# Kernel tuning notes

Hardware: AMD Instinct MI355X
Metric: run time of the kernel (lower is better)

Reference implementation:

```python
import jax, jax.numpy as jnp
import numpy as np

H = 16
D_MODEL = 1024
D_K = D_MODEL // H
SEQ = 2048
BATCH = 2


def setup_inputs() -> dict:
    key = jax.random.key(0)
    ks = jax.random.split(key, 11)
    s = 1.0 / np.sqrt(D_MODEL)
    inp = {
        "query": jax.random.normal(ks[0], (SEQ, BATCH, D_MODEL), jnp.float32),
        "key_": jax.random.normal(ks[1], (SEQ, BATCH, D_MODEL), jnp.float32),
        "value": jax.random.normal(ks[2], (SEQ, BATCH, D_MODEL), jnp.float32),
        "Wq": jax.random.uniform(ks[3], (D_MODEL, D_MODEL), jnp.float32, -s, s),
        "bq": jax.random.uniform(ks[4], (D_MODEL,), jnp.float32, -s, s),
        "Wk": jax.random.uniform(ks[5], (D_MODEL, D_MODEL), jnp.float32, -s, s),
        "bk": jax.random.uniform(ks[6], (D_MODEL,), jnp.float32, -s, s),
        "Wv": jax.random.uniform(ks[7], (D_MODEL, D_MODEL), jnp.float32, -s, s),
        "bv": jax.random.uniform(ks[8], (D_MODEL,), jnp.float32, -s, s),
        "Wo": jax.random.uniform(ks[9], (D_MODEL, D_MODEL), jnp.float32, -s, s),
        "bo": jax.random.uniform(ks[10], (D_MODEL,), jnp.float32, -s, s),
    }
    return inp


def _mha(query, key_, value, Wq, bq, Wk, bk, Wv, bv, Wo, bo):
    S, B, D = query.shape
    # torch Linear: x @ W.T + b; then view(S,B,h,dk).transpose(0,2) -> [h,B,S,dk]
    def proj(x, W, b):
        return jnp.transpose((x @ W.T + b).reshape(S, B, H, D_K), (2, 1, 0, 3))

    q = proj(query, Wq, bq)   # [h, b, S, dk]
    k = proj(key_, Wk, bk)
    v = proj(value, Wv, bv)

    scores = jnp.einsum("hbqd,hbkd->hbqk", q, k) / jnp.sqrt(
        jnp.asarray(D_K, q.dtype)
    )  # [h, b, S, S]
    p_attn = jax.nn.softmax(scores, axis=-1)  # dropout p=0.0 -> identity
    x = jnp.einsum("hbqk,hbkd->hbqd", p_attn, v)  # [h, b, S, dk]
    x = jnp.transpose(x, (2, 1, 0, 3)).reshape(S, B, D)  # back to [S, B, D]
    return x @ Wo.T + bo


def reference(query, key_, value, Wq, bq, Wk, bk, Wv, bv, Wo, bo):
    return _mha(query, key_, value, Wq, bq, Wk, bk, Wv, bv, Wo, bo)
```

## Files before the change

kernel.cpp:

```cpp
#include <hip/hip_runtime.h>

#define SEQ   2048
#define BATCH 2
#define DM    1024
#define NH    16
#define DKD   64
#define MROWS (SEQ*BATCH)

#define QSCALE 0.18033688011112042f

using bf16x8 = __attribute__((ext_vector_type(8))) __bf16;
using bf16x4 = __attribute__((ext_vector_type(4))) __bf16;
using bf16x2 = __attribute__((ext_vector_type(2))) __bf16;
using f32x4  = __attribute__((ext_vector_type(4))) float;

__device__ __forceinline__ void gld_lds16(const __bf16* g, __bf16* l) {
  __builtin_amdgcn_global_load_lds(
      (__attribute__((address_space(1))) void*)(g),
      (__attribute__((address_space(3))) void*)(l), 16, 0, 0);
}

__global__ __launch_bounds__(256) void cvt_all(
    const float* __restrict__ s0, const float* __restrict__ s1,
    const float* __restrict__ s2, const float* __restrict__ s3,
    const float* __restrict__ s4, const float* __restrict__ s5,
    const float* __restrict__ s6,
    __bf16* __restrict__ d0, __bf16* __restrict__ d1, __bf16* __restrict__ d2,
    __bf16* __restrict__ d3, __bf16* __restrict__ d4, __bf16* __restrict__ d5,
    __bf16* __restrict__ d6, int n_big, int n_small) {
  int y = blockIdx.y;
  const float* s; __bf16* d;
  switch (y) {
    case 0: s = s0; d = d0; break;
    case 1: s = s1; d = d1; break;
    case 2: s = s2; d = d2; break;
    case 3: s = s3; d = d3; break;
    case 4: s = s4; d = d4; break;
    case 5: s = s5; d = d5; break;
    default: s = s6; d = d6; break;
  }
  int n = (y < 3) ? n_big : n_small;
  int i = (blockIdx.x * 256 + threadIdx.x) * 8;
  if (i >= n) return;
  const float4* sp = (const float4*)(s + i);
  float4 a = sp[0], b = sp[1];
  bf16x8 v;
  v[0]=(__bf16)a.x; v[1]=(__bf16)a.y; v[2]=(__bf16)a.z; v[3]=(__bf16)a.w;
  v[4]=(__bf16)b.x; v[5]=(__bf16)b.y; v[6]=(__bf16)b.z; v[7]=(__bf16)b.w;
  *(bf16x8*)(d + i) = v;
}

__device__ __forceinline__ void gemm_core(const __bf16* __restrict__ A,
                                          const __bf16* __restrict__ Bt,
                                          __bf16* Ash, __bf16* Bsh,
                                          f32x4 acc[4][4], int m0, int n0) {
  const int K = DM;
  int tid = threadIdx.x;
  int lane = tid & 63, quad = lane >> 4, l16 = lane & 15;
  int w = tid >> 6;
  int wm = (w & 1) * 64, wn = (w >> 1) * 64;
  for (int k0 = 0; k0 < K; k0 += 32) {
    __syncthreads();
#pragma unroll
    for (int it = 0; it < 2; ++it) {
      int c   = tid + it * 256;
      int row = c >> 2, ko = (c & 3) * 8;
      int base = (tid - lane + it * 256) * 8;
      gld_lds16(A  + (size_t)(m0 + row) * K + k0 + ko, Ash + base);
      gld_lds16(Bt + (size_t)(n0 + row) * K + k0 + ko, Bsh + base);
    }
    __syncthreads();
    bf16x8 af[4], bfr[4];
#pragma unroll
    for (int mi = 0; mi < 4; mi++)
      af[mi] = *(const bf16x8*)&Ash[(wm + mi * 16 + l16) * 32 + quad * 8];
#pragma unroll
    for (int ni = 0; ni < 4; ni++)
      bfr[ni] = *(const bf16x8*)&Bsh[(wn + ni * 16 + l16) * 32 + quad * 8];
#pragma unroll
    for (int mi = 0; mi < 4; mi++)
#pragma unroll
      for (int ni = 0; ni < 4; ni++)
        acc[mi][ni] = __builtin_amdgcn_mfma_f32_16x16x32_bf16(
            af[mi], bfr[ni], acc[mi][ni], 0, 0, 0);
  }
}

__global__ __launch_bounds__(256, 3) void gemm_qkv(
    const __bf16* __restrict__ Xq, const __bf16* __restrict__ Xk,
    const __bf16* __restrict__ Xv, const __bf16* __restrict__ Wqkv,
    const float* __restrict__ bqp, const float* __restrict__ bkp,
    const float* __restrict__ bvp,
    __bf16* __restrict__ Qb, __bf16* __restrict__ Kb, __bf16* __restrict__ Vt) {
  __shared__ __bf16 Ash[128 * 32], Bsh[128 * 32];
  __shared__ __bf16 Esh[4][16 * 72];
  int z = blockIdx.z;
  const __bf16* A   = (z == 0) ? Xq : (z == 1) ? Xk : Xv;
  const __bf16* Bt  = Wqkv + (size_t)z * (DM * DM);
  const float* bias = (z == 0) ? bqp : (z == 1) ? bkp : bvp;
  int m0 = blockIdx.y * 128, n0 = blockIdx.x * 128;
  f32x4 acc[4][4] = {};
  gemm_core(A, Bt, Ash, Bsh, acc, m0, n0);

  int tid = threadIdx.x, lane = tid & 63, quad = lane >> 4, l16 = lane & 15;
  int w = tid >> 6, wm = (w & 1) * 64, wn = (w >> 1) * 64;
  __bf16* E = Esh[w];
  int n_base = n0 + wn;
  int hh = n_base >> 6;
  float scale = (z == 0) ? QSCALE : 1.0f;
  float bb[4];
#pragma unroll
  for (int ni = 0; ni < 4; ni++) bb[ni] = bias[n_base + ni * 16 + l16] * scale;

  if (z == 2) {
#pragma unroll
    for (int ni = 0; ni < 4; ni++) {
#pragma unroll
      for (int mi = 0; mi < 4; mi++) {
        int s0 = mi * 8 + quad * 2;
        bf16x2 p0, p1;
        p0[0] = (__bf16)(acc[mi][ni][0] + bb[ni]);
        p0[1] = (__bf16)(acc[mi][ni][2] + bb[ni]);
        p1[0] = (__bf16)(acc[mi][ni][1] + bb[ni]);
        p1[1] = (__bf16)(acc[mi][ni][3] + bb[ni]);
        *(bf16x2*)&E[l16 * 72 + s0]      = p0;
        *(bf16x2*)&E[l16 * 72 + 32 + s0] = p1;
      }
      asm volatile("s_waitcnt lgkmcnt(0)" ::: "memory");
#pragma unroll
      for (int pass = 0; pass < 2; pass++) {
        int ddl = pass * 8 + (lane >> 3);
        int col = (lane & 7) * 8;
        bf16x8 v = *(const bf16x8*)&E[ddl * 72 + col];
        int b2 = col >> 5, sl = col & 31;
        int dd = ni * 16 + ddl;
        int sg = ((m0 + wm) >> 1) + sl;
        *(bf16x8*)&Vt[(((size_t)hh * BATCH + b2) * DKD + dd) * SEQ + sg] = v;
      }
      asm volatile("s_waitcnt lgkmcnt(0)" ::: "memory");
    }
  } else {
    __bf16* Out = (z == 0) ? Qb : Kb;
#pragma unroll
    for (int mi = 0; mi < 4; mi++) {
#pragma unroll
      for (int ni = 0; ni < 4; ni++)
#pragma unroll
        for (int r = 0; r < 4; r++)
          E[(quad * 4 + r) * 72 + ni * 16 + l16] =
              (__bf16)fmaf(acc[mi][ni][r], scale, bb[ni]);
      asm volatile("s_waitcnt lgkmcnt(0)" ::: "memory");
#pragma unroll
      for (int pass = 0; pass < 2; pass++) {
        int row16 = pass * 8 + (lane >> 3);
        int coll  = (lane & 7) * 8;
        bf16x8 v = *(const bf16x8*)&E[row16 * 72 + coll];
        int m = m0 + wm + mi * 16 + row16;
        int s = m >> 1, b2 = m & 1;
        *(bf16x8*)&Out[(((size_t)hh * BATCH + b2) * SEQ + s) * DKD + coll] = v;
      }
      asm volatile("s_waitcnt lgkmcnt(0)" ::: "memory");
    }
  }
}

__global__ __launch_bounds__(256, 3) void gemm_out(
    const __bf16* __restrict__ A, const __bf16* __restrict__ Bt,
    const float* __restrict__ bias, float* __restrict__ out) {
  __shared__ __bf16 Ash[64 * 32], Bsh[128 * 32];
  const int K = DM;
  int m0 = blockIdx.y * 64, n0 = blockIdx.x * 128;
  int tid = threadIdx.x;
  int lane = tid & 63, quad = lane >> 4, l16 = lane & 15;
  int w = tid >> 6;
  int wm = (w & 1) * 32, wn = (w >> 1) * 64;
  f32x4 acc[2][4] = {};
  for (int k0 = 0; k0 < K; k0 += 32) {
    __syncthreads();
    {
      int c = tid;
      int row = c >> 2, ko = (c & 3) * 8;
      gld_lds16(A + (size_t)(m0 + row) * K + k0 + ko,
                Ash + (tid - lane) * 8);
    }
#pragma unroll
    for (int it = 0; it < 2; ++it) {
      int c = tid + it * 256;
      int row = c >> 2, ko = (c & 3) * 8;
      gld_lds16(Bt + (size_t)(n0 + row) * K + k0 + ko,
                Bsh + (tid - lane + it * 256) * 8);
    }
    __syncthreads();
    bf16x8 af[2], bfr[4];
#pragma unroll
    for (int mi = 0; mi < 2; mi++)
      af[mi] = *(const bf16x8*)&Ash[(wm + mi * 16 + l16) * 32 + quad * 8];
#pragma unroll
    for (int ni = 0; ni < 4; ni++)
      bfr[ni] = *(const bf16x8*)&Bsh[(wn + ni * 16 + l16) * 32 + quad * 8];
#pragma unroll
    for (int mi = 0; mi < 2; mi++)
#pragma unroll
      for (int ni = 0; ni < 4; ni++)
        acc[mi][ni] = __builtin_amdgcn_mfma_f32_16x16x32_bf16(
            af[mi], bfr[ni], acc[mi][ni], 0, 0, 0);
  }
#pragma unroll
  for (int ni = 0; ni < 4; ni++) {
    int n = n0 + wn + ni * 16 + l16;
    float bb = bias[n];
#pragma unroll
    for (int mi = 0; mi < 2; mi++) {
#pragma unroll
      for (int r = 0; r < 4; r++) {
        int m = m0 + wm + mi * 16 + quad * 4 + r;
        out[(size_t)m * DM + n] = acc[mi][ni][r] + bb;
      }
    }
  }
}

__global__ __launch_bounds__(512, 4) void flash_attn(
    const __bf16* __restrict__ Qg, const __bf16* __restrict__ Kg,
    const __bf16* __restrict__ Vtg, __bf16* __restrict__ Xa) {
  __shared__ __bf16 Ksh[2][64 * 64];
  __shared__ __bf16 Vsh[2][64 * 64];
  __shared__ __bf16 Psh[8][16 * 64];
  int tid = threadIdx.x, w = tid >> 6, lane = tid & 63;
  int quad = lane >> 4, l16 = lane & 15, sw = l16 & 7;
  int n = blockIdx.x;
  int hb = n & 31, qi = n >> 5;
  int h = hb >> 1, b = hb & 1, q0 = qi * 128;
  size_t hboff = ((size_t)h * BATCH + b) * SEQ * DKD;
  const __bf16* Qp = Qg + hboff;
  const __bf16* Kp = Kg + hboff;
  const __bf16* Vp = Vtg + hboff;
  __bf16* Pw = Psh[w];

  bf16x8 qf[2];
#pragma unroll
  for (int kk = 0; kk < 2; kk++)
    qf[kk] = *(const bf16x8*)(
        Qp + (size_t)(q0 + w * 16 + l16) * DKD + kk * 32 + quad * 8);

  f32x4 o[4] = {};
  float l_ = 0.f;

  {
    int c = tid;
    int r = c >> 3, pp = c & 7;
    int off = (pp ^ (r & 7)) << 3;
    gld_lds16(Kp + (size_t)r * DKD + off, Ksh[0] + c * 8);
    gld_lds16(Vp + (size_t)r * SEQ + off, Vsh[0] + c * 8);
  }

  for (int t = 0; t < SEQ / 64; ++t) {
    __syncthreads();
    if (t + 1 < SEQ / 64) {
      int k0n = (t + 1) * 64, bn = (t + 1) & 1;
      int c = tid;
      int r = c >> 3, pp = c & 7;
      int off = (pp ^ (r & 7)) << 3;
      gld_lds16(Kp + (size_t)(k0n + r) * DKD + off, Ksh[bn] + c * 8);
      gld_lds16(Vp + (size_t)r * SEQ + k0n + off, Vsh[bn] + c * 8);
    }
    const __bf16* Kb_ = Ksh[t & 1];
    const __bf16* Vb_ = Vsh[t & 1];

    f32x4 sc[4];
#pragma unroll
    for (int ji = 0; ji < 4; ji++) {
      int rr = ji * 16 + l16;
      bf16x8 kf0 = *(const bf16x8*)&Kb_[rr * 64 + ((quad ^ sw) << 3)];
      bf16x8 kf1 = *(const bf16x8*)&Kb_[rr * 64 + (((4 + quad) ^ sw) << 3)];
      f32x4 t2 = {0.f, 0.f, 0.f, 0.f};
      t2 = __builtin_amdgcn_mfma_f32_16x16x32_bf16(kf0, qf[0], t2, 0, 0, 0);
      t2 = __builtin_amdgcn_mfma_f32_16x16x32_bf16(kf1, qf[1], t2, 0, 0, 0);
      sc[ji] = t2;
    }

#pragma unroll
    for (int ji = 0; ji < 4; ji++) {
      bf16x4 pk;
#pragma unroll
      for (int r = 0; r < 4; r++) {
        float pv = exp2f(sc[ji][r]);
        l_ += pv;
        pk[r] = (__bf16)pv;
      }
      *(bf16x4*)&Pw[l16 * 64 +
                    (((ji * 2 + (quad >> 1)) ^ sw) << 3) + ((quad & 1) << 2)] = pk;
    }

#pragma unroll
    for (int kk = 0; kk < 2; kk++) {
      bf16x8 pa = *(const bf16x8*)&Pw[l16 * 64 + (((kk * 4 + quad) ^ sw) << 3)];
#pragma unroll
      for (int ni = 0; ni < 4; ni++) {
        int rr = ni * 16 + l16;
        bf16x8 vb = *(const bf16x8*)&Vb_[rr * 64 + (((kk * 4 + quad) ^ sw) << 3)];
        o[ni] = __builtin_amdgcn_mfma_f32_16x16x32_bf16(pa, vb, o[ni], 0, 0, 0);
      }
    }
  }

  l_ += __shfl_xor(l_, 16, 64);
  l_ += __shfl_xor(l_, 32, 64);
  l_ = 1.0f / l_;
#pragma unroll
  for (int r = 0; r < 4; r++) {
    float li = __shfl(l_, quad * 4 + r, 64);
    int q = q0 + w * 16 + quad * 4 + r;
#pragma unroll
    for (int ni = 0; ni < 4; ni++) {
      int d = ni * 16 + l16;
      Xa[((size_t)q * BATCH + b) * DM + h * DKD + d] =
          (__bf16)(o[ni][r] * li);
    }
  }
}

extern "C" void kernel_launch(void* const* d_in, const int* in_sizes, int n_in,
                              void* d_out, int out_size, void* d_ws,
                              size_t ws_size, hipStream_t stream) {
  (void)in_sizes; (void)n_in; (void)out_size; (void)ws_size;
  const float* query = (const float*)d_in[0];
  const float* key_  = (const float*)d_in[1];
  const float* value = (const float*)d_in[2];
  const float* Wq = (const float*)d_in[3];
  const float* bq = (const float*)d_in[4];
  const float* Wk = (const float*)d_in[5];
  const float* bk = (const float*)d_in[6];
  const float* Wv = (const float*)d_in[7];
  const float* bv = (const float*)d_in[8];
  const float* Wo = (const float*)d_in[9];
  const float* bo = (const float*)d_in[10];

  const size_t NX = (size_t)MROWS * DM;
  const size_t NW = (size_t)DM * DM;
  __bf16* p    = (__bf16*)d_ws;
  __bf16* Xq   = p; p += NX;
  __bf16* Xk   = p; p += NX;
  __bf16* Xv   = p; p += NX;
  __bf16* Wqkv = p; p += 3 * NW;
  __bf16* Wob  = p; p += NW;
  __bf16* Qb   = p; p += NX;
  __bf16* Kb   = p; p += NX;
  __bf16* Vt   = p; p += NX;
  __bf16* Xa   = Xq;

  cvt_all<<<dim3((unsigned)(NX / 2048), 7), 256, 0, stream>>>(
      query, key_, value, Wq, Wk, Wv, Wo,
      Xq, Xk, Xv, Wqkv, Wqkv + NW, Wqkv + 2 * NW, Wob, (int)NX, (int)NW);

  gemm_qkv<<<dim3(DM / 128, MROWS / 128, 3), 256, 0, stream>>>(
      Xq, Xk, Xv, Wqkv, bq, bk, bv, Qb, Kb, Vt);
  flash_attn<<<dim3(512), 512, 0, stream>>>(Qb, Kb, Vt, Xa);
  gemm_out<<<dim3(DM / 128, MROWS / 64), 256, 0, stream>>>(
      Xa, Wob, bo, (float*)d_out);
}
```

Baseline: 228.6 us.

## Double GEMM K-tile to 64 with XOR-swizzled LDS; add setprio in attention

Both GEMM kernels now stage 64-wide K slices per iteration instead of 32. The LDS tiles use an XOR swizzle to avoid bank conflicts, and each slice runs two MFMA sub-steps. This halves the number of barriers and loop iterations per tile, but doubles the LDS footprint, which may limit occupancy. The flash attention kernel also wraps its MFMA phases in s_setprio and splits the row-sum accumulator into two, which shortens the dependency chain.

```diff
diff --git a/kernel.cpp b/kernel.cpp
--- a/kernel.cpp
+++ b/kernel.cpp
@@ -56,33 +56,39 @@
                                           f32x4 acc[4][4], int m0, int n0) {
   const int K = DM;
   int tid = threadIdx.x;
-  int lane = tid & 63, quad = lane >> 4, l16 = lane & 15;
+  int lane = tid & 63, quad = lane >> 4, l16 = lane & 15, sw = l16 & 7;
   int w = tid >> 6;
   int wm = (w & 1) * 64, wn = (w >> 1) * 64;
-  for (int k0 = 0; k0 < K; k0 += 32) {
-    __syncthreads();
-#pragma unroll
-    for (int it = 0; it < 2; ++it) {
+  for (int k0 = 0; k0 < K; k0 += 64) {
+    __syncthreads();
+#pragma unroll
+    for (int it = 0; it < 4; ++it) {
       int c   = tid + it * 256;
-      int row = c >> 2, ko = (c & 3) * 8;
+      int row = c >> 3, pp = c & 7;
+      int ko  = (pp ^ (row & 7)) << 3;
       int base = (tid - lane + it * 256) * 8;
       gld_lds16(A  + (size_t)(m0 + row) * K + k0 + ko, Ash + base);
       gld_lds16(Bt + (size_t)(n0 + row) * K + k0 + ko, Bsh + base);
     }
     __syncthreads();
-    bf16x8 af[4], bfr[4];
-#pragma unroll
-    for (int mi = 0; mi < 4; mi++)
-      af[mi] = *(const bf16x8*)&Ash[(wm + mi * 16 + l16) * 32 + quad * 8];
-#pragma unroll
-    for (int ni = 0; ni < 4; ni++)
-      bfr[ni] = *(const bf16x8*)&Bsh[(wn + ni * 16 + l16) * 32 + quad * 8];
-#pragma unroll
-    for (int mi = 0; mi < 4; mi++)
+#pragma unroll
+    for (int kk = 0; kk < 2; ++kk) {
+      bf16x8 af[4], bfr[4];
+#pragma unroll
+      for (int mi = 0; mi < 4; mi++)
+        af[mi] = *(const bf16x8*)&Ash[(wm + mi * 16 + l16) * 64 +
+                                      (((kk * 4 + quad) ^ sw) << 3)];
 #pragma unroll
       for (int ni = 0; ni < 4; ni++)
-        acc[mi][ni] = __builtin_amdgcn_mfma_f32_16x16x32_bf16(
-            af[mi], bfr[ni], acc[mi][ni], 0, 0, 0);
+        bfr[ni] = *(const bf16x8*)&Bsh[(wn + ni * 16 + l16) * 64 +
+                                       (((kk * 4 + quad) ^ sw) << 3)];
+#pragma unroll
+      for (int mi = 0; mi < 4; mi++)
+#pragma unroll
+        for (int ni = 0; ni < 4; ni++)
+          acc[mi][ni] = __builtin_amdgcn_mfma_f32_16x16x32_bf16(
+              af[mi], bfr[ni], acc[mi][ni], 0, 0, 0);
+    }
   }
 }
 
@@ -92,7 +98,7 @@
     const float* __restrict__ bqp, const float* __restrict__ bkp,
     const float* __restrict__ bvp,
     __bf16* __restrict__ Qb, __bf16* __restrict__ Kb, __bf16* __restrict__ Vt) {
-  __shared__ __bf16 Ash[128 * 32], Bsh[128 * 32];
+  __shared__ __bf16 Ash[128 * 64], Bsh[128 * 64];
   __shared__ __bf16 Esh[4][16 * 72];
   int z = blockIdx.z;
   const __bf16* A   = (z == 0) ? Xq : (z == 1) ? Xk : Xv;
@@ -167,43 +173,51 @@
 __global__ __launch_bounds__(256, 3) void gemm_out(
     const __bf16* __restrict__ A, const __bf16* __restrict__ Bt,
     const float* __restrict__ bias, float* __restrict__ out) {
-  __shared__ __bf16 Ash[64 * 32], Bsh[128 * 32];
+  __shared__ __bf16 Ash[64 * 64], Bsh[128 * 64];
   const int K = DM;
   int m0 = blockIdx.y * 64, n0 = blockIdx.x * 128;
   int tid = threadIdx.x;
-  int lane = tid & 63, quad = lane >> 4, l16 = lane & 15;
+  int lane = tid & 63, quad = lane >> 4, l16 = lane & 15, sw = l16 & 7;
   int w = tid >> 6;
   int wm = (w & 1) * 32, wn = (w >> 1) * 64;
   f32x4 acc[2][4] = {};
-  for (int k0 = 0; k0 < K; k0 += 32) {
-    __syncthreads();
-    {
-      int c = tid;
-      int row = c >> 2, ko = (c & 3) * 8;
-      gld_lds16(A + (size_t)(m0 + row) * K + k0 + ko,
-                Ash + (tid - lane) * 8);
-    }
+  for (int k0 = 0; k0 < K; k0 += 64) {
+    __syncthreads();
 #pragma unroll
     for (int it = 0; it < 2; ++it) {
       int c = tid + it * 256;
-      int row = c >> 2, ko = (c & 3) * 8;
+      int row = c >> 3, pp = c & 7;
+      int ko = (pp ^ (row & 7)) << 3;
+      gld_lds16(A + (size_t)(m0 + row) * K + k0 + ko,
+                Ash + (tid - lane + it * 256) * 8);
+    }
+#pragma unroll
+    for (int it = 0; it < 4; ++it) {
+      int c = tid + it * 256;
+      int row = c >> 3, pp = c & 7;
+      int ko = (pp ^ (row & 7)) << 3;
       gld_lds16(Bt + (size_t)(n0 + row) * K + k0 + ko,
                 Bsh + (tid - lane + it * 256) * 8);
     }
     __syncthreads();
-    bf16x8 af[2], bfr[4];
-#pragma unroll
-    for (int mi = 0; mi < 2; mi++)
-      af[mi] = *(const bf16x8*)&Ash[(wm + mi * 16 + l16) * 32 + quad * 8];
-#pragma unroll
-    for (int ni = 0; ni < 4; ni++)
-      bfr[ni] = *(const bf16x8*)&Bsh[(wn + ni * 16 + l16) * 32 + quad * 8];
-#pragma unroll
-    for (int mi = 0; mi < 2; mi++)
+#pragma unroll
+    for (int kk = 0; kk < 2; ++kk) {
+      bf16x8 af[2], bfr[4];
+#pragma unroll
+      for (int mi = 0; mi < 2; mi++)
+        af[mi] = *(const bf16x8*)&Ash[(wm + mi * 16 + l16) * 64 +
+                                      (((kk * 4 + quad) ^ sw) << 3)];
 #pragma unroll
       for (int ni = 0; ni < 4; ni++)
-        acc[mi][ni] = __builtin_amdgcn_mfma_f32_16x16x32_bf16(
-            af[mi], bfr[ni], acc[mi][ni], 0, 0, 0);
+        bfr[ni] = *(const bf16x8*)&Bsh[(wn + ni * 16 + l16) * 64 +
+                                       (((kk * 4 + quad) ^ sw) << 3)];
+#pragma unroll
+      for (int mi = 0; mi < 2; mi++)
+#pragma unroll
+        for (int ni = 0; ni < 4; ni++)
+          acc[mi][ni] = __builtin_amdgcn_mfma_f32_16x16x32_bf16(
+              af[mi], bfr[ni], acc[mi][ni], 0, 0, 0);
+    }
   }
 #pragma unroll
   for (int ni = 0; ni < 4; ni++) {
@@ -244,7 +258,7 @@
         Qp + (size_t)(q0 + w * 16 + l16) * DKD + kk * 32 + quad * 8);
 
   f32x4 o[4] = {};
-  float l_ = 0.f;
+  float l_a = 0.f, l_b = 0.f;
 
   {
     int c = tid;
@@ -268,6 +282,7 @@
     const __bf16* Vb_ = Vsh[t & 1];
 
     f32x4 sc[4];
+    __builtin_amdgcn_s_setprio(1);
 #pragma unroll
     for (int ji = 0; ji < 4; ji++) {
       int rr = ji * 16 + l16;
@@ -278,6 +293,7 @@
       t2 = __builtin_amdgcn_mfma_f32_16x16x32_bf16(kf1, qf[1], t2, 0, 0, 0);
       sc[ji] = t2;
     }
+    __builtin_amdgcn_s_setprio(0);
 
 #pragma unroll
     for (int ji = 0; ji < 4; ji++) {
@@ -285,13 +301,14 @@
 #pragma unroll
       for (int r = 0; r < 4; r++) {
         float pv = exp2f(sc[ji][r]);
-        l_ += pv;
+        if (ji & 1) l_b += pv; else l_a += pv;
         pk[r] = (__bf16)pv;
       }
       *(bf16x4*)&Pw[l16 * 64 +
                     (((ji * 2 + (quad >> 1)) ^ sw) << 3) + ((quad & 1) << 2)] = pk;
     }
 
+    __builtin_amdgcn_s_setprio(1);
 #pragma unroll
     for (int kk = 0; kk < 2; kk++) {
       bf16x8 pa = *(const bf16x8*)&Pw[l16 * 64 + (((kk * 4 + quad) ^ sw) << 3)];
@@ -302,8 +319,10 @@
         o[ni] = __builtin_amdgcn_mfma_f32_16x16x32_bf16(pa, vb, o[ni], 0, 0, 0);
       }
     }
-  }
-
+    __builtin_amdgcn_s_setprio(0);
+  }
+
+  float l_ = l_a + l_b;
   l_ += __shfl_xor(l_, 16, 64);
   l_ += __shfl_xor(l_, 32, 64);
   l_ = 1.0f / l_;
```

New measurement: 224.9 us. No clear change (-1.6%).
